# Performance work log

Measured on AMD Instinct MI355X. Metric: run time of the kernel, lower is better.

Reference implementation:

```python
import jax, jax.numpy as jnp
import numpy as np

D, D_r, G, I = 1024, 64, 2, 2
Ng = D // G  # 512
F = (2 * I + 1) * G  # 10 gathered features per group
BATCH = 4096


def _make_idx():
    # Replicates the torch index construction (modulo-wrapped ring neighbors).
    base = 2 * (np.arange(-I, I + 1).reshape(-1, 1) % Ng)  # (2I+1, 1)
    base = np.concatenate([base, base + 1], axis=1).reshape(-1)  # (2*(2I+1),) == (F,)
    idx = np.stack([(base + 2 * i) % D for i in range(Ng)], axis=0)  # (Ng, F)
    return jnp.asarray(idx, dtype=jnp.int64)


def setup_inputs() -> dict:
    key = jax.random.key(0)
    k1, k2, k3, k4 = jax.random.split(key, 4)
    x = jax.random.normal(k1, (BATCH, D), dtype=jnp.float32)
    # torch.nn.Linear init scale ~ 1/sqrt(fan_in)
    W_in = jax.random.normal(k2, (D_r, F), dtype=jnp.float32) / np.sqrt(F)
    b_in = jax.random.normal(k3, (D_r,), dtype=jnp.float32) / np.sqrt(F)
    W_out = jax.random.normal(k4, (G, D_r), dtype=jnp.float32) / np.sqrt(D_r)
    return {"x": x, "W_in": W_in, "b_in": b_in, "W_out": W_out, "idx": _make_idx()}


def reference(x, W_in, b_in, W_out, idx):
    # gather ring neighbors: [B, Ng, F]
    g = x[..., idx]
    # inner linear + tanh: [B, Ng, D_r]
    h = jnp.tanh(jnp.einsum('bnf,rf->bnr', g, W_in) + b_in)
    # outer linear (no bias): [B, Ng, G] -> reshape to [B, D]
    y = jnp.einsum('bnr,gr->bng', h, W_out).reshape(x.shape)
    return x + y
```

## Files before the change

### kernel.cpp

```cpp
#include <hip/hip_runtime.h>

typedef __fp16 half8    __attribute__((ext_vector_type(8)));
typedef __fp16 half2v   __attribute__((ext_vector_type(2)));
typedef float  float16v __attribute__((ext_vector_type(16)));
typedef unsigned uint4v __attribute__((ext_vector_type(4)));

#if defined(__has_builtin) && __has_builtin(__builtin_amdgcn_fdot2)
#define DOT2(a, b, c) __builtin_amdgcn_fdot2((a), (b), (c), false)
#else
#define DOT2(a, b, c) ((c) + (float)(a).x * (float)(b).x + (float)(a).y * (float)(b).y)
#endif

__device__ __forceinline__ unsigned pack2(float a, float b) {
    return __builtin_bit_cast(unsigned, __builtin_amdgcn_cvt_pkrtz(a, b));
}

__global__ __launch_bounds__(512, 4) void pe_ilp(
    const float* __restrict__ x, const float* __restrict__ W_in,
    const float* __restrict__ b_in, const float* __restrict__ W_out,
    float* __restrict__ out, int batch)
{
    __shared__ __align__(16) unsigned sU[2][528];

    const int t    = threadIdx.x;
    const int lane = t & 63;
    const int wv   = t >> 6;
    const int n32  = lane & 31;
    const int g    = lane >> 5;
    const int row0 = 2 * blockIdx.x;

    #pragma unroll
    for (int r = 0; r < 2; ++r) {
        const float* xr = x + (size_t)(row0 + r) * 1024;
        const float2 v = reinterpret_cast<const float2*>(xr)[t];
        const unsigned pkv = pack2(v.x, v.y);
        sU[r][2 + t] = pkv;
        if (t < 2)        sU[r][514 + t] = pkv;
        else if (t < 16)  sU[r][512 + t] = 0u;
        if (t >= 510)     sU[r][t - 510] = pkv;
    }

    half8 Af[2];
    #pragma unroll
    for (int mf = 0; mf < 2; ++mf) {
        const int R = 32 * mf + n32;
        #pragma unroll
        for (int j = 0; j < 8; ++j) {
            const int k = 8 * g + j;
            float w = 0.f;
            if (k < 10) w = W_in[R * 10 + k];
            else if (k == 10) w = b_in[R];
            Af[mf][j] = (__fp16)w;
        }
    }
    half2v Wp[2][8][2];
    #pragma unroll
    for (int mf = 0; mf < 2; ++mf)
        #pragma unroll
        for (int p = 0; p < 8; ++p) {
            const int R = 32 * mf + ((p & 1) << 1) + 8 * (p >> 1) + 4 * g;
            #pragma unroll
            for (int o = 0; o < 2; ++o)
                Wp[mf][p][o] = __builtin_amdgcn_cvt_pkrtz(W_out[o * 64 + R], W_out[o * 64 + R + 1]);
        }

    __syncthreads();

    const half2v C0 = {(__fp16)0.98931f,     (__fp16)0.98931f};
    const half2v C1 = {(__fp16)-0.26964f,    (__fp16)-0.26964f};
    const half2v C2 = {(__fp16)0.054759f,    (__fp16)0.054759f};
    const half2v C3 = {(__fp16)-0.0057126f,  (__fp16)-0.0057126f};
    const half2v C4 = {(__fp16)0.00022867f,  (__fp16)0.00022867f};
    const half2v HI = {(__fp16)3.0f,  (__fp16)3.0f};
    const half2v LO = {(__fp16)-3.0f, (__fp16)-3.0f};
    const float16v Zacc = {};

    auto epilogue = [&](const float16v& Da, const float16v& Db,
                        int n, unsigned hp2, float* orow) {
        float a00 = 0.f, a01 = 0.f, a10 = 0.f, a11 = 0.f;
        #pragma unroll
        for (int mf = 0; mf < 2; ++mf) {
            const float16v& D = mf ? Db : Da;
            #pragma unroll
            for (int p = 0; p < 8; ++p) {
                half2v zt = __builtin_amdgcn_cvt_pkrtz(D[2 * p], D[2 * p + 1]);
                zt = __builtin_elementwise_min(__builtin_elementwise_max(zt, LO), HI);
                const half2v z2 = zt * zt;
                half2v P = C4;
                P = P * z2 + C3;
                P = P * z2 + C2;
                P = P * z2 + C1;
                P = P * z2 + C0;
                const half2v th = zt * P;
                if (p & 1) {
                    a10 = DOT2(th, Wp[mf][p][0], a10);
                    a11 = DOT2(th, Wp[mf][p][1], a11);
                } else {
                    a00 = DOT2(th, Wp[mf][p][0], a00);
                    a01 = DOT2(th, Wp[mf][p][1], a01);
                }
            }
        }
        const half2v pk = __builtin_amdgcn_cvt_pkrtz(a00 + a10, a01 + a11);
        const int   pi  = __shfl_xor(__builtin_bit_cast(int, pk), 32, 64);
        const half2v sum = pk + __builtin_bit_cast(half2v, pi);
        if (lane < 32) {
            const half2v o2 = sum + __builtin_bit_cast(half2v, hp2);
            float2 o;
            o.x = (float)o2.x;
            o.y = (float)o2.y;
            *reinterpret_cast<float2*>(orow + 2 * n) = o;
        }
    };

    #pragma unroll
    for (int r = 0; r < 2; ++r) {
        if (row0 + r >= batch) break;
        const unsigned* su = sU[r];
        float* orow = out + (size_t)(row0 + r) * 1024;

        const int n0 = wv * 64 + n32;
        const int n1 = n0 + 32;
        const int d0 = n0 + 4 * g;
        const int d1 = n1 + 4 * g;

        unsigned h00 = su[d0], h01 = su[d0 + 1], h02 = su[d0 + 2], h03 = su[d0 + 3];
        unsigned h10 = su[d1], h11 = su[d1 + 1], h12 = su[d1 + 2], h13 = su[d1 + 3];
        const unsigned res0 = h02, res1 = h12;
        if (g) {
            h01 = 0x00003C00u; h02 = 0u; h03 = 0u;
            h11 = 0x00003C00u; h12 = 0u; h13 = 0u;
        }
        const uint4v u0 = {h00, h01, h02, h03};
        const uint4v u1 = {h10, h11, h12, h13};
        const half8 Bf0 = __builtin_bit_cast(half8, u0);
        const half8 Bf1 = __builtin_bit_cast(half8, u1);

        const float16v D00 = __builtin_amdgcn_mfma_f32_32x32x16_f16(Af[0], Bf0, Zacc, 0, 0, 0);
        const float16v D01 = __builtin_amdgcn_mfma_f32_32x32x16_f16(Af[1], Bf0, Zacc, 0, 0, 0);
        const float16v D10 = __builtin_amdgcn_mfma_f32_32x32x16_f16(Af[0], Bf1, Zacc, 0, 0, 0);
        const float16v D11 = __builtin_amdgcn_mfma_f32_32x32x16_f16(Af[1], Bf1, Zacc, 0, 0, 0);

        epilogue(D00, D01, n0, res0, orow);
        epilogue(D10, D11, n1, res1, orow);
    }
}

extern "C" void kernel_launch(void* const* d_in, const int* in_sizes, int n_in,
                              void* d_out, int out_size, void* d_ws, size_t ws_size,
                              hipStream_t stream) {
    const float* x     = (const float*)d_in[0];
    const float* W_in  = (const float*)d_in[1];
    const float* b_in  = (const float*)d_in[2];
    const float* W_out = (const float*)d_in[3];
    float* out = (float*)d_out;
    const int batch = in_sizes[0] / 1024;
    const int grid  = (batch + 1) / 2;
    pe_ilp<<<grid, 512, 0, stream>>>(x, W_in, b_in, W_out, out, batch);
}
```

Measured before the change: 106.5 us.

## Split into pack kernel writing fp16 rows and weights to workspace, then compute kernel

Adds a pre-pass kernel that converts each x row to packed fp16 with ring-wrap padding and pre-packs the W_in/b_in and W_out fragments into the workspace. The main kernel then reads those fragments directly from global memory with vector loads instead of staging through LDS and rebuilding weights per block. It processes one row per 256-thread block. The aim is to remove per-block weight conversion and the LDS barrier, at the cost of an extra launch and a round trip through the workspace.

```diff
diff --git a/kernel.cpp b/kernel.cpp
--- a/kernel.cpp
+++ b/kernel.cpp
@@ -11,60 +11,87 @@
 #define DOT2(a, b, c) ((c) + (float)(a).x * (float)(b).x + (float)(a).y * (float)(b).y)
 #endif
 
+#define XPK_STRIDE 528
+
 __device__ __forceinline__ unsigned pack2(float a, float b) {
     return __builtin_bit_cast(unsigned, __builtin_amdgcn_cvt_pkrtz(a, b));
 }
+__device__ __forceinline__ half2v h2(unsigned u) {
+    return __builtin_bit_cast(half2v, u);
+}
 
-__global__ __launch_bounds__(512, 4) void pe_ilp(
+
+__global__ __launch_bounds__(256) void pe_pack(
     const float* __restrict__ x, const float* __restrict__ W_in,
     const float* __restrict__ b_in, const float* __restrict__ W_out,
-    float* __restrict__ out, int batch)
+    unsigned* __restrict__ ws, int batch)
 {
-    __shared__ __align__(16) unsigned sU[2][528];
+    const int b = blockIdx.x;
+    const int t = threadIdx.x;
+    if (b < batch) {
+        const float* xr = x + (size_t)b * 1024;
+        unsigned* dst = ws + (size_t)b * XPK_STRIDE;
+        const float2 v0 = reinterpret_cast<const float2*>(xr)[t];
+        const float2 v1 = reinterpret_cast<const float2*>(xr)[t + 256];
+        dst[2 + t]       = pack2(v0.x, v0.y);
+        dst[258 + t]     = pack2(v1.x, v1.y);
+        if (t < 2)    dst[514 + t] = pack2(xr[2 * t], xr[2 * t + 1]);
+        if (t >= 254) dst[t - 254] = pack2(v1.x, v1.y);
+    } else {
+        unsigned* wt = ws + (size_t)batch * XPK_STRIDE;
+        {
+            const int a  = t >> 1;
+            const int mf = a & 1, n32 = (a >> 1) & 31, g = a >> 6;
+            const int R  = 32 * mf + n32, j0 = 4 * (t & 1);
+            float v[4];
+            #pragma unroll
+            for (int jj = 0; jj < 4; ++jj) {
+                const int k = 8 * g + j0 + jj;
+                v[jj] = (k < 10) ? W_in[R * 10 + k] : (k == 10 ? b_in[R] : 0.f);
+            }
+            wt[a * 4 + 2 * (t & 1) + 0] = pack2(v[0], v[1]);
+            wt[a * 4 + 2 * (t & 1) + 1] = pack2(v[2], v[3]);
+        }
+        if (t < 64) {
+            const int o = t & 1, p = (t >> 1) & 7, mf = (t >> 4) & 1, g = t >> 5;
+            const int R = 32 * mf + ((p & 1) << 1) + 8 * (p >> 1) + 4 * g;
+            wt[512 + t] = pack2(W_out[o * 64 + R], W_out[o * 64 + R + 1]);
+        }
+    }
+}
 
+__global__ __launch_bounds__(256) void pe_main(
+    const unsigned* __restrict__ ws, float* __restrict__ out, int batch)
+{
     const int t    = threadIdx.x;
     const int lane = t & 63;
     const int wv   = t >> 6;
     const int n32  = lane & 31;
     const int g    = lane >> 5;
-    const int row0 = 2 * blockIdx.x;
+    const int row  = blockIdx.x;
 
-    #pragma unroll
-    for (int r = 0; r < 2; ++r) {
-        const float* xr = x + (size_t)(row0 + r) * 1024;
-        const float2 v = reinterpret_cast<const float2*>(xr)[t];
-        const unsigned pkv = pack2(v.x, v.y);
-        sU[r][2 + t] = pkv;
-        if (t < 2)        sU[r][514 + t] = pkv;
-        else if (t < 16)  sU[r][512 + t] = 0u;
-        if (t >= 510)     sU[r][t - 510] = pkv;
-    }
+    const unsigned* su = ws + (size_t)row * XPK_STRIDE;
+    const unsigned* wt = ws + (size_t)batch * XPK_STRIDE;
 
     half8 Af[2];
     #pragma unroll
     for (int mf = 0; mf < 2; ++mf) {
-        const int R = 32 * mf + n32;
-        #pragma unroll
-        for (int j = 0; j < 8; ++j) {
-            const int k = 8 * g + j;
-            float w = 0.f;
-            if (k < 10) w = W_in[R * 10 + k];
-            else if (k == 10) w = b_in[R];
-            Af[mf][j] = (__fp16)w;
-        }
+        const uint4v q = *reinterpret_cast<const uint4v*>(wt + ((g * 32 + n32) * 2 + mf) * 4);
+        Af[mf] = __builtin_bit_cast(half8, q);
     }
     half2v Wp[2][8][2];
     #pragma unroll
-    for (int mf = 0; mf < 2; ++mf)
+    for (int mf = 0; mf < 2; ++mf) {
+        const int base = 512 + (g * 2 + mf) * 16;
         #pragma unroll
-        for (int p = 0; p < 8; ++p) {
-            const int R = 32 * mf + ((p & 1) << 1) + 8 * (p >> 1) + 4 * g;
-            #pragma unroll
-            for (int o = 0; o < 2; ++o)
-                Wp[mf][p][o] = __builtin_amdgcn_cvt_pkrtz(W_out[o * 64 + R], W_out[o * 64 + R + 1]);
+        for (int c = 0; c < 4; ++c) {
+            const uint4v q = *reinterpret_cast<const uint4v*>(wt + base + 4 * c);
+            Wp[mf][2 * c][0]     = h2(q.x);
+            Wp[mf][2 * c][1]     = h2(q.y);
+            Wp[mf][2 * c + 1][0] = h2(q.z);
+            Wp[mf][2 * c + 1][1] = h2(q.w);
         }
-
-    __syncthreads();
+    }
 
     const half2v C0 = {(__fp16)0.98931f,     (__fp16)0.98931f};
     const half2v C1 = {(__fp16)-0.26964f,    (__fp16)-0.26964f};
@@ -75,8 +102,22 @@
     const half2v LO = {(__fp16)-3.0f, (__fp16)-3.0f};
     const float16v Zacc = {};
 
-    auto epilogue = [&](const float16v& Da, const float16v& Db,
-                        int n, unsigned hp2, float* orow) {
+    float* orow = out + (size_t)row * 1024;
+
+    #pragma unroll
+    for (int it = 0; it < 4; ++it) {
+        const int n  = (wv * 4 + it) * 32 + n32;
+        const int d0 = n + 4 * g;
+
+        unsigned h0 = su[d0], h1 = su[d0 + 1], h2u = su[d0 + 2], h3 = su[d0 + 3];
+        const unsigned res = h2u;
+        if (g) { h1 = 0x00003C00u; h2u = 0u; h3 = 0u; }
+        const uint4v uB = {h0, h1, h2u, h3};
+        const half8 Bf = __builtin_bit_cast(half8, uB);
+
+        const float16v Da = __builtin_amdgcn_mfma_f32_32x32x16_f16(Af[0], Bf, Zacc, 0, 0, 0);
+        const float16v Db = __builtin_amdgcn_mfma_f32_32x32x16_f16(Af[1], Bf, Zacc, 0, 0, 0);
+
         float a00 = 0.f, a01 = 0.f, a10 = 0.f, a11 = 0.f;
         #pragma unroll
         for (int mf = 0; mf < 2; ++mf) {
@@ -101,48 +142,18 @@
                 }
             }
         }
+
         const half2v pk = __builtin_amdgcn_cvt_pkrtz(a00 + a10, a01 + a11);
         const int   pi  = __shfl_xor(__builtin_bit_cast(int, pk), 32, 64);
         const half2v sum = pk + __builtin_bit_cast(half2v, pi);
+
         if (lane < 32) {
-            const half2v o2 = sum + __builtin_bit_cast(half2v, hp2);
+            const half2v o2 = sum + h2(res);
             float2 o;
             o.x = (float)o2.x;
             o.y = (float)o2.y;
             *reinterpret_cast<float2*>(orow + 2 * n) = o;
         }
-    };
-
-    #pragma unroll
-    for (int r = 0; r < 2; ++r) {
-        if (row0 + r >= batch) break;
-        const unsigned* su = sU[r];
-        float* orow = out + (size_t)(row0 + r) * 1024;
-
-        const int n0 = wv * 64 + n32;
-        const int n1 = n0 + 32;
-        const int d0 = n0 + 4 * g;
-        const int d1 = n1 + 4 * g;
-
-        unsigned h00 = su[d0], h01 = su[d0 + 1], h02 = su[d0 + 2], h03 = su[d0 + 3];
-        unsigned h10 = su[d1], h11 = su[d1 + 1], h12 = su[d1 + 2], h13 = su[d1 + 3];
-        const unsigned res0 = h02, res1 = h12;
-        if (g) {
-            h01 = 0x00003C00u; h02 = 0u; h03 = 0u;
-            h11 = 0x00003C00u; h12 = 0u; h13 = 0u;
-        }
-        const uint4v u0 = {h00, h01, h02, h03};
-        const uint4v u1 = {h10, h11, h12, h13};
-        const half8 Bf0 = __builtin_bit_cast(half8, u0);
-        const half8 Bf1 = __builtin_bit_cast(half8, u1);
-
-        const float16v D00 = __builtin_amdgcn_mfma_f32_32x32x16_f16(Af[0], Bf0, Zacc, 0, 0, 0);
-        const float16v D01 = __builtin_amdgcn_mfma_f32_32x32x16_f16(Af[1], Bf0, Zacc, 0, 0, 0);
-        const float16v D10 = __builtin_amdgcn_mfma_f32_32x32x16_f16(Af[0], Bf1, Zacc, 0, 0, 0);
-        const float16v D11 = __builtin_amdgcn_mfma_f32_32x32x16_f16(Af[1], Bf1, Zacc, 0, 0, 0);
-
-        epilogue(D00, D01, n0, res0, orow);
-        epilogue(D10, D11, n1, res1, orow);
     }
 }
 
@@ -155,6 +166,7 @@
     const float* W_out = (const float*)d_in[3];
     float* out = (float*)d_out;
     const int batch = in_sizes[0] / 1024;
-    const int grid  = (batch + 1) / 2;
-    pe_ilp<<<grid, 512, 0, stream>>>(x, W_in, b_in, W_out, out, batch);
+    unsigned* ws = (unsigned*)d_ws;
+    pe_pack<<<batch + 1, 256, 0, stream>>>(x, W_in, b_in, W_out, ws, batch);
+    pe_main<<<batch, 256, 0, stream>>>(ws, out, batch);
 }
```

Result: faster. 104.1 us (-2.3%).
